# Performance work log

Hardware: AMD Instinct MI355X
Metric: run time of the kernel (lower is better)

## Reference

```python
import jax, jax.numpy as jnp
import numpy as np
from jax import lax

B, L, T = 16, 512, 128
V, D = 21128, 512


def setup_inputs() -> dict:
    key = jax.random.key(0)
    ks = jax.random.split(key, 24)
    s = 0.05
    p = lambda k, shape: jax.random.normal(k, shape, jnp.float32) * s
    return {
        'document_input_ids': jax.random.randint(ks[0], (B, L), 0, V),
        'summary_input_ids': jax.random.randint(ks[1], (B, T), 0, V),
        'E': p(ks[2], (V, D)),
        'Wih_f': p(ks[3], (4 * D, D)), 'Whh_f': p(ks[4], (4 * D, D)),
        'bih_f': p(ks[5], (4 * D,)), 'bhh_f': p(ks[6], (4 * D,)),
        'Wih_b': p(ks[7], (4 * D, D)), 'Whh_b': p(ks[8], (4 * D, D)),
        'bih_b': p(ks[9], (4 * D,)), 'bhh_b': p(ks[10], (4 * D,)),
        'fc_W': p(ks[11], (D, 2 * D)), 'fc_b': p(ks[12], (D,)),
        'attn_W': p(ks[13], (D, 3 * D)), 'attn_b': p(ks[14], (D,)),
        'v_w': p(ks[15], (D,)),
        'dWih': p(ks[16], (4 * D, 3 * D)),
        'dbih': p(ks[17], (4 * D,)), 'dbhh': p(ks[18], (4 * D,)),
        'dfc_W': p(ks[19], (V, 4 * D)), 'dfc_b': p(ks[20], (V,)),
    }


def _lstm_dir(x, Wih, Whh, bih, bhh, reverse):
    # x: (B, L, Din) -> outputs (B, L, D) plus final hidden (B, D)
    xg = jnp.einsum('bld,gd->blg', x, Wih) + bih + bhh  # precompute input gates

    def step(carry, xt):
        h, c = carry
        g = xt + h @ Whh.T
        i, f, gg, o = jnp.split(g, 4, axis=-1)  # PyTorch gate order i,f,g,o
        i = jax.nn.sigmoid(i); f = jax.nn.sigmoid(f)
        gg = jnp.tanh(gg); o = jax.nn.sigmoid(o)
        c = f * c + i * gg
        h = o * jnp.tanh(c)
        return (h, c), h

    h0 = jnp.zeros((x.shape[0], Whh.shape[1]), x.dtype)
    (hT, _), hs = lax.scan(step, (h0, h0), jnp.swapaxes(xg, 0, 1), reverse=reverse)
    return jnp.swapaxes(hs, 0, 1), hT


def reference(document_input_ids, summary_input_ids, E,
              Wih_f, Whh_f, bih_f, bhh_f,
              Wih_b, Whh_b, bih_b, bhh_b,
              fc_W, fc_b, attn_W, attn_b, v_w,
              dWih, dbih, dbhh, dfc_W, dfc_b):
    # --- encoder (BiLSTM over document; dropout is identity at eval) ---
    emb = E[document_input_ids]                       # (B, L, D)
    enc_f, h_f = _lstm_dir(emb, Wih_f, Whh_f, bih_f, bhh_f, reverse=False)
    enc_b, h_b = _lstm_dir(emb, Wih_b, Whh_b, bih_b, bhh_b, reverse=True)
    enc = jnp.concatenate([enc_f, enc_b], axis=-1)    # (B, L, 2D)
    hidden = jnp.tanh(jnp.concatenate([h_f, h_b], axis=-1) @ fc_W.T + fc_b)  # (B, D)

    # --- Bahdanau attention, computed once (as in the original forward) ---
    bsz, dlen = enc.shape[0], enc.shape[1]
    hrep = jnp.broadcast_to(hidden[:, None, :], (bsz, dlen, hidden.shape[-1]))
    energy = jnp.tanh(jnp.concatenate([hrep, enc], axis=2) @ attn_W.T + attn_b)
    att = energy @ v_w                                 # (B, L)
    mask = document_input_ids != 0
    att = jnp.where(mask, att, jnp.float32(-1e10))
    a = jax.nn.softmax(att, axis=1)
    weighted = jnp.einsum('bl,ble->be', a, enc)        # (B, 2D), constant over steps

    # --- decoder: teacher forcing; d_lstm gets a fresh zero state each step,
    # so all T-1 steps are independent and fully vectorized ---
    toks = summary_input_ids[:, :-1]                   # inputs for t = 1..T-1
    emb_s = E[toks]                                    # (B, T-1, D)
    w_b = jnp.broadcast_to(weighted[:, None, :], (bsz, toks.shape[1], weighted.shape[-1]))
    x = jnp.concatenate([emb_s, w_b], axis=2)          # (B, T-1, 3D)
    g = jnp.einsum('btd,gd->btg', x, dWih) + dbih + dbhh
    i, f, gg, o = jnp.split(g, 4, axis=-1)
    c = jax.nn.sigmoid(i) * jnp.tanh(gg)               # h_prev = c_prev = 0
    h = jax.nn.sigmoid(o) * jnp.tanh(c)                # (B, T-1, D)
    pred = jnp.einsum('btd,vd->btv', jnp.concatenate([h, w_b, emb_s], axis=2), dfc_W) + dfc_b
    logits = jnp.concatenate([jnp.zeros((bsz, 1, pred.shape[-1]), pred.dtype), pred], axis=1)
    logits = jnp.transpose(logits, (0, 2, 1))          # (B, V, T) as in the torch code

    # --- CrossEntropyLoss over all positions (incl. the zero-logit t=0) ---
    logp = jax.nn.log_softmax(logits, axis=1)
    nll = -jnp.take_along_axis(logp, summary_input_ids[:, None, :], axis=1).squeeze(1)
    loss = nll.mean()
    return logits, loss
```

## Files before the change

kernel.cpp:

```cpp
#include <hip/hip_runtime.h>
#include <math.h>

typedef __attribute__((ext_vector_type(8))) short bf16x8;
typedef __attribute__((ext_vector_type(4))) float f32x4;
typedef unsigned int u32;
typedef unsigned short u16;
typedef unsigned long long u64;

#define BB 16
#define LL 512
#define TT 128
#define VV 21128
#define DD 512

__device__ __forceinline__ float b2f(u16 h){ return __uint_as_float(((u32)h) << 16); }
__device__ __forceinline__ u16 f2bf(float x){
    u32 u = __float_as_uint(x);
    return (u16)((u + 0x7fffu + ((u >> 16) & 1u)) >> 16);
}
__device__ __forceinline__ float sigf(float x){ return 1.0f / (1.0f + __expf(-x)); }
__device__ __forceinline__ bf16x8 pack8(float4 a, float4 b){
    bf16x8 r;
    r[0]=(short)f2bf(a.x); r[1]=(short)f2bf(a.y); r[2]=(short)f2bf(a.z); r[3]=(short)f2bf(a.w);
    r[4]=(short)f2bf(b.x); r[5]=(short)f2bf(b.y); r[6]=(short)f2bf(b.z); r[7]=(short)f2bf(b.w);
    return r;
}

__global__ void kz(u32* p, int n){
    int i = blockIdx.x * 256 + threadIdx.x;
    if (i < n) p[i] = 0u;
}

__global__ void k_embed(const int* __restrict__ doc, const float* __restrict__ E,
                        u16* __restrict__ emb2){
    int r = blockIdx.x;
    int lane = threadIdx.x;
    int l = r >> 4, b = r & 15;
    int tok = doc[b * LL + l];
    const float* src = E + (size_t)tok * DD + lane * 8;
    float4 a = *(const float4*)(src);
    float4 c = *(const float4*)(src + 4);
    *(bf16x8*)(emb2 + (size_t)r * DD + lane * 8) = pack8(a, c);
}

template<int MODE>
__global__ __launch_bounds__(256) void k_gemm(
    const u16* __restrict__ A, const float* __restrict__ Bt, void* __restrict__ Out,
    const float* __restrict__ b1, const float* __restrict__ b2, int M, int N, int K)
{
    __shared__ u16 smem[17408];
    u16* sA = smem;
    u16* sB = smem + 128 * 56;
    int tid = threadIdx.x;
    int nb = blockIdx.x, mb = blockIdx.y;
    int wv = tid >> 6, lane = tid & 63;
    int wm = wv >> 1, wn = wv & 1;
    int lrow = lane & 15, quad = lane >> 4;
    f32x4 acc[4][4] = {};
    int kt_n = K >> 5;
    for (int kt = 0; kt < kt_n; ++kt){
        int k0 = kt << 5;
        bf16x8 va[2];
        u64 qb[4];
        #pragma unroll
        for (int h = 0; h < 2; ++h){
            int c = tid + (h << 8);
            int row = c >> 2, c4 = c & 3;
            va[h] = *(const bf16x8*)(A + (size_t)(mb * 128 + row) * K + k0 + c4 * 8);
        }
        #pragma unroll
        for (int h = 0; h < 4; ++h){
            int c = tid + (h << 8);
            int row = c >> 3, seg = c & 7;
            int rb = nb * 128 + row; rb = rb < N ? rb : N - 1;
            float4 v = *(const float4*)(Bt + (size_t)rb * K + k0 + seg * 4);
            qb[h] = (u64)f2bf(v.x) | ((u64)f2bf(v.y) << 16) |
                    ((u64)f2bf(v.z) << 32) | ((u64)f2bf(v.w) << 48);
        }
        __syncthreads();
        #pragma unroll
        for (int h = 0; h < 2; ++h){
            int c = tid + (h << 8);
            int row = c >> 2, c4 = c & 3;
            *(bf16x8*)(sA + row * 56 + c4 * 8) = va[h];
        }
        #pragma unroll
        for (int h = 0; h < 4; ++h){
            int c = tid + (h << 8);
            int row = c >> 3, seg = c & 7;
            *(u64*)(sB + row * 56 + seg * 4) = qb[h];
        }
        __syncthreads();
        bf16x8 af[4], bfr[4];
        #pragma unroll
        for (int i = 0; i < 4; ++i){
            af[i]  = *(const bf16x8*)(sA + (wm * 64 + i * 16 + lrow) * 56 + quad * 8);
            bfr[i] = *(const bf16x8*)(sB + (wn * 64 + i * 16 + lrow) * 56 + quad * 8);
        }
        #pragma unroll
        for (int i = 0; i < 4; ++i)
            #pragma unroll
            for (int j = 0; j < 4; ++j)
                acc[i][j] = __builtin_amdgcn_mfma_f32_16x16x32_bf16(af[i], bfr[j], acc[i][j], 0, 0, 0);
    }

    if (MODE == 0 || MODE == 1){
        u16* O = (u16*)Out;
        #pragma unroll
        for (int i = 0; i < 4; ++i){
            int rowb = mb * 128 + wm * 64 + i * 16 + quad * 4;
            #pragma unroll
            for (int j = 0; j < 4; ++j){
                int col = nb * 128 + wn * 64 + j * 16 + lrow;
                float bias = b1[col] + (b2 ? b2[col] : 0.0f);
                #pragma unroll
                for (int r = 0; r < 4; ++r){
                    float v = acc[i][j][r] + bias;
                    if (MODE == 1) v = tanhf(v);
                    O[(size_t)(rowb + r) * N + col] = f2bf(v);
                }
            }
        }
    } else {
        float* Of = (float*)Out;
        float* lds_f = (float*)smem;
        #pragma unroll
        for (int h = 0; h < 2; ++h){
            __syncthreads();
            if (wn == h){
                #pragma unroll
                for (int j = 0; j < 4; ++j){
                    int nl = j * 16 + lrow;
                    int vg = nb * 128 + h * 64 + nl;
                    float bias = (vg < VV) ? b1[vg] : 0.0f;
                    #pragma unroll
                    for (int i = 0; i < 4; ++i){
                        #pragma unroll
                        for (int r = 0; r < 4; ++r){
                            int tl = wm * 64 + i * 16 + quad * 4 + r;
                            lds_f[nl * 132 + tl] = (tl == 0) ? 0.0f : (acc[i][j][r] + bias);
                        }
                    }
                }
            }
            __syncthreads();
            int vloc = tid >> 2, seg = tid & 3;
            int ng = nb * 128 + h * 64 + vloc;
            if (ng < VV){
                float4* dst = (float4*)(Of + ((size_t)mb * VV + ng) * TT + seg * 32);
                const float4* src = (const float4*)(lds_f + vloc * 132 + seg * 32);
                #pragma unroll
                for (int q = 0; q < 8; ++q) dst[q] = src[q];
            }
        }
    }
}

__global__ __launch_bounds__(256) void k_lstm(
    const u16* __restrict__ xg_f, const u16* __restrict__ xg_b,
    const float* __restrict__ Whh_f, const float* __restrict__ Whh_b,
    u16* __restrict__ hist_f, u16* __restrict__ hist_b,
    u32* __restrict__ hbuf, u32* __restrict__ cnt)
{
    __shared__ u16 h_lds[16 * 544];
    __shared__ float g_lds[4 * 16 * 16];
    int tid = threadIdx.x;
    int dir = blockIdx.x >> 5;
    int slice = blockIdx.x & 31;
    int d0 = slice << 4;
    int wv = tid >> 6, lane = tid & 63;
    int lrow = lane & 15, quad = lane >> 4;
    const u16* xg  = dir ? xg_b : xg_f;
    const float* Whh = dir ? Whh_b : Whh_f;
    u16* hist = dir ? hist_b : hist_f;

    bf16x8 bfrag[16];
    {
        int nrow = (wv << 9) + d0 + lrow;
        const float* wp = Whh + (size_t)nrow * DD;
        #pragma unroll
        for (int kb = 0; kb < 16; ++kb){
            float4 x0 = *(const float4*)(wp + kb * 32 + quad * 8);
            float4 x1 = *(const float4*)(wp + kb * 32 + quad * 8 + 4);
            bfrag[kb] = pack8(x0, x1);
        }
    }
    float c_reg = 0.0f;
    int um = tid >> 4, udc = tid & 15;

    for (int s = 0; s < LL; ++s){
        int t = dir ? (LL - 1 - s) : s;
        int rp = s & 1, wpar = rp ^ 1;
        u32* hb_r = hbuf + ((dir * 2 + rp) << 12);
        #pragma unroll
        for (int j = 0; j < 16; ++j){
            u32 u = __hip_atomic_load(hb_r + (j << 8) + tid, __ATOMIC_RELAXED, __HIP_MEMORY_SCOPE_AGENT);
            *(u32*)(h_lds + j * 544 + (tid << 1)) = u;
        }
        __syncthreads();
        f32x4 acc = {};
        #pragma unroll
        for (int kb = 0; kb < 16; ++kb){
            bf16x8 af = *(const bf16x8*)(h_lds + lrow * 544 + kb * 32 + quad * 8);
            acc = __builtin_amdgcn_mfma_f32_16x16x32_bf16(af, bfrag[kb], acc, 0, 0, 0);
        }
        {
            const u16* xp = xg + ((size_t)(t << 4)) * 2048 + (wv << 9) + d0 + lrow;
            #pragma unroll
            for (int r = 0; r < 4; ++r){
                int m = (quad << 2) + r;
                float gv = acc[r] + b2f(xp[(size_t)m * 2048]);
                g_lds[(wv << 8) + (m << 4) + lrow] = gv;
            }
        }
        __syncthreads();
        {
            float gi = g_lds[(0 << 8) + (um << 4) + udc];
            float gf = g_lds[(1 << 8) + (um << 4) + udc];
            float gg = g_lds[(2 << 8) + (um << 4) + udc];
            float go = g_lds[(3 << 8) + (um << 4) + udc];
            float cv = sigf(gf) * c_reg + sigf(gi) * tanhf(gg);
            c_reg = cv;
            float h = sigf(go) * tanhf(cv);
            float ho = __shfl_xor(h, 1);
            if ((tid & 1) == 0){
                u32 u = ((u32)f2bf(ho) << 16) | (u32)f2bf(h);
                u32* hb_w = hbuf + ((dir * 2 + wpar) << 12);
                __hip_atomic_store(hb_w + (um << 8) + ((d0 + udc) >> 1), u, __ATOMIC_RELAXED, __HIP_MEMORY_SCOPE_AGENT);
                *(u32*)(hist + ((size_t)(t * 16 + um)) * DD + d0 + udc) = u;
            }
        }
        __syncthreads();
        if (tid == 0){
            __hip_atomic_fetch_add(cnt, 1, __ATOMIC_ACQ_REL, __HIP_MEMORY_SCOPE_AGENT);
            int target = (s + 1) << 6;
            while (__hip_atomic_load(cnt, __ATOMIC_ACQUIRE, __HIP_MEMORY_SCOPE_AGENT) < target)
                __builtin_amdgcn_s_sleep(2);
        }
        __syncthreads();
    }
}

__global__ void k_fc(const u16* __restrict__ hist_f, const u16* __restrict__ hist_b,
                     const float* __restrict__ fcW, const float* __restrict__ fcB,
                     u16* __restrict__ hidden){
    int idx = blockIdx.x * 256 + threadIdx.x;
    int b = idx >> 9, n = idx & 511;
    const u16* hf = hist_f + (size_t)(511 * 16 + b) * DD;
    const u16* hb = hist_b + (size_t)b * DD;
    const float* w = fcW + (size_t)n * 1024;
    float sacc = 0.0f;
    for (int k = 0; k < 512; ++k) sacc += b2f(hf[k]) * w[k];
    for (int k = 0; k < 512; ++k) sacc += b2f(hb[k]) * w[512 + k];
    hidden[b * 512 + n] = f2bf(tanhf(sacc + fcB[n]));
}

__global__ void k_packatt(const u16* __restrict__ hidden, const u16* __restrict__ hist_f,
                          const u16* __restrict__ hist_b, u16* __restrict__ X){
    int r = blockIdx.x;
    int b = r >> 9, l = r & 511;
    u16* xr = X + (size_t)r * 1536;
    const u16* hf = hist_f + (size_t)(l * 16 + b) * DD;
    const u16* hb = hist_b + (size_t)(l * 16 + b) * DD;
    const u16* hd = hidden + b * 512;
    for (int j = threadIdx.x; j < 512; j += 256){
        xr[j] = hd[j];
        xr[512 + j] = hf[j];
        xr[1024 + j] = hb[j];
    }
}

__global__ void k_att(const u16* __restrict__ energy, const float* __restrict__ vw,
                      const int* __restrict__ doc, float* __restrict__ att){
    int r = blockIdx.x * 4 + (threadIdx.x >> 6);
    int lane = threadIdx.x & 63;
    bf16x8 e = *(const bf16x8*)(energy + (size_t)r * 512 + lane * 8);
    float4 v0 = *(const float4*)(vw + lane * 8);
    float4 v1 = *(const float4*)(vw + lane * 8 + 4);
    float sacc = b2f((u16)e[0]) * v0.x + b2f((u16)e[1]) * v0.y +
                 b2f((u16)e[2]) * v0.z + b2f((u16)e[3]) * v0.w +
                 b2f((u16)e[4]) * v1.x + b2f((u16)e[5]) * v1.y +
                 b2f((u16)e[6]) * v1.z + b2f((u16)e[7]) * v1.w;
    #pragma unroll
    for (int o = 1; o < 64; o <<= 1) sacc += __shfl_xor(sacc, o);
    if (lane == 0){
        int b = r >> 9, l = r & 511;
        att[r] = (doc[b * 512 + l] != 0) ? sacc : -1e10f;
    }
}

__global__ __launch_bounds__(256) void k_smw(const float* __restrict__ att,
                                             const u16* __restrict__ hist_f,
                                             const u16* __restrict__ hist_b,
                                             float* __restrict__ weighted){
    __shared__ float sa[512];
    __shared__ float red[256];
    int b = blockIdx.x, tid = threadIdx.x;
    float a0 = att[b * 512 + tid], a1 = att[b * 512 + 256 + tid];
    red[tid] = fmaxf(a0, a1); __syncthreads();
    for (int o = 128; o > 0; o >>= 1){ if (tid < o) red[tid] = fmaxf(red[tid], red[tid + o]); __syncthreads(); }
    float mx = red[0]; __syncthreads();
    float e0 = __expf(a0 - mx), e1 = __expf(a1 - mx);
    red[tid] = e0 + e1; __syncthreads();
    for (int o = 128; o > 0; o >>= 1){ if (tid < o) red[tid] += red[tid + o]; __syncthreads(); }
    float inv = 1.0f / red[0];
    sa[tid] = e0 * inv; sa[256 + tid] = e1 * inv;
    __syncthreads();
    #pragma unroll
    for (int ch = 0; ch < 4; ++ch){
        int e = (ch << 8) + tid;
        const u16* src = (e < 512) ? (hist_f + b * DD + e) : (hist_b + b * DD + (e - 512));
        float acc = 0.0f;
        for (int l = 0; l < 512; ++l) acc += sa[l] * b2f(src[(size_t)l * 16 * DD]);
        weighted[b * 1024 + e] = acc;
    }
}

__global__ void k_packdec(const int* __restrict__ sids, const float* __restrict__ E,
                          const float* __restrict__ weighted,
                          u16* __restrict__ X_dec, u16* __restrict__ X_pred){
    int r = blockIdx.x;
    int b = r >> 7, t = r & 127;
    u16* xd = X_dec + (size_t)r * 1536;
    u16* xp = X_pred + (size_t)r * 2048;
    const float* er = (t > 0) ? (E + (size_t)sids[b * 128 + t - 1] * DD) : (const float*)0;
    for (int j = threadIdx.x; j < 512; j += 256){
        u16 v = (t > 0) ? f2bf(er[j]) : (u16)0;
        xd[j] = v; xp[1536 + j] = v;
    }
    for (int j = threadIdx.x; j < 1024; j += 256){
        u16 wv = f2bf(weighted[b * 1024 + j]);
        xd[512 + j] = wv; xp[512 + j] = wv;
    }
}

__global__ void k_gate(const u16* __restrict__ g, u16* __restrict__ X_pred){
    int idx = blockIdx.x * 256 + threadIdx.x;
    int r = idx >> 9, d = idx & 511;
    const u16* gr = g + (size_t)r * 2048;
    float gi = b2f(gr[d]), gg = b2f(gr[1024 + d]), go = b2f(gr[1536 + d]);
    float c = sigf(gi) * tanhf(gg);
    X_pred[(size_t)r * 2048 + d] = f2bf(sigf(go) * tanhf(c));
}

__global__ void k_lossp(const float* __restrict__ out, float* __restrict__ part){
    int b = blockIdx.x >> 5, ch = blockIdx.x & 31;
    int t = threadIdx.x;
    int v0 = ch * 661, v1 = v0 + 661; if (v1 > VV) v1 = VV;
    const float* col = out + (size_t)b * VV * TT + t;
    float m = -1e30f, sacc = 0.0f;
    for (int v = v0; v < v1; ++v){
        float x = col[(size_t)v * TT];
        float nm = fmaxf(m, x);
        sacc = sacc * __expf(m - nm) + __expf(x - nm);
        m = nm;
    }
    float2* p = (float2*)part;
    p[((b * 32 + ch) << 7) + t] = make_float2(m, sacc);
}

__global__ __launch_bounds__(256) void k_lossm(const float* __restrict__ part,
                                               const float* __restrict__ out,
                                               const int* __restrict__ sids,
                                               float* __restrict__ loss_out){
    __shared__ float red[256];
    int tid = threadIdx.x;
    float local = 0.0f;
    #pragma unroll
    for (int p8 = 0; p8 < 8; ++p8){
        int pair = (p8 << 8) + tid;
        int b = pair >> 7, t = pair & 127;
        const float2* pp = (const float2*)part + ((size_t)(b * 32) << 7) + t;
        float M = -1e30f;
        for (int c = 0; c < 32; ++c) M = fmaxf(M, pp[c << 7].x);
        float S = 0.0f;
        for (int c = 0; c < 32; ++c){ float2 q = pp[c << 7]; S += q.y * __expf(q.x - M); }
        float logZ = M + __logf(S);
        int tgt = sids[b * 128 + t];
        float x = out[(size_t)b * VV * TT + (size_t)tgt * TT + t];
        local += (logZ - x);
    }
    red[tid] = local; __syncthreads();
    for (int o = 128; o > 0; o >>= 1){ if (tid < o) red[tid] += red[tid + o]; __syncthreads(); }
    if (tid == 0) loss_out[0] = red[0] / 2048.0f;
}

extern "C" void kernel_launch(void* const* d_in, const int* in_sizes, int n_in,
                              void* d_out, int out_size, void* d_ws, size_t ws_size,
                              hipStream_t stream)
{
    const int*   doc  = (const int*)d_in[0];
    const int*   sids = (const int*)d_in[1];
    const float* E    = (const float*)d_in[2];
    const float* WihF = (const float*)d_in[3];
    const float* WhhF = (const float*)d_in[4];
    const float* bihF = (const float*)d_in[5];
    const float* bhhF = (const float*)d_in[6];
    const float* WihB = (const float*)d_in[7];
    const float* WhhB = (const float*)d_in[8];
    const float* bihB = (const float*)d_in[9];
    const float* bhhB = (const float*)d_in[10];
    const float* fcW  = (const float*)d_in[11];
    const float* fcB  = (const float*)d_in[12];
    const float* attW = (const float*)d_in[13];
    const float* attB = (const float*)d_in[14];
    const float* vw   = (const float*)d_in[15];
    const float* dWih = (const float*)d_in[16];
    const float* dbih = (const float*)d_in[17];
    const float* dbhh = (const float*)d_in[18];
    const float* dfcW = (const float*)d_in[19];
    const float* dfcB = (const float*)d_in[20];
    float* out = (float*)d_out;

    char* ws = (char*)d_ws;
    const size_t EMB2 = 0;
    const size_t XG   = EMB2 + 8388608ull;
    const size_t XGB  = XG   + 33554432ull;
    const size_t HHF  = XGB  + 33554432ull;
    const size_t HHB  = HHF  + 8388608ull;
    const size_t HBUF = HHB  + 8388608ull;
    const size_t HID  = HBUF + 66560ull;
    const size_t XATT = XG;
    const size_t ENER = XATT + 25165824ull;
    const size_t ATT  = ENER + 8388608ull;
    const size_t WEI  = ATT  + 32768ull;
    const size_t XDEC = WEI  + 65536ull;
    const size_t GDEC = XDEC + 6291456ull;
    const size_t XPRD = GDEC + 8388608ull;
    const size_t PART = XPRD + 8388608ull;

    u16* emb2  = (u16*)(ws + EMB2);
    u16* xgf   = (u16*)(ws + XG);
    u16* xgb   = (u16*)(ws + XGB);
    u16* hhf   = (u16*)(ws + HHF);
    u16* hhb   = (u16*)(ws + HHB);
    u32* hbuf  = (u32*)(ws + HBUF);
    u16* hid   = (u16*)(ws + HID);
    u16* xatt  = (u16*)(ws + XATT);
    u16* ener  = (u16*)(ws + ENER);
    float* att = (float*)(ws + ATT);
    float* wei = (float*)(ws + WEI);
    u16* xdec  = (u16*)(ws + XDEC);
    u16* gdec  = (u16*)(ws + GDEC);
    u16* xprd  = (u16*)(ws + XPRD);
    float* part= (float*)(ws + PART);

    (void)in_sizes; (void)n_in; (void)out_size; (void)ws_size;

    kz<<<dim3(65), dim3(256), 0, stream>>>(hbuf, 16512);
    k_embed<<<dim3(8192), dim3(64), 0, stream>>>(doc, E, emb2);
    k_gemm<0><<<dim3(16, 64), dim3(256), 0, stream>>>(emb2, WihF, (void*)xgf, bihF, bhhF, 8192, 2048, 512);
    k_gemm<0><<<dim3(16, 64), dim3(256), 0, stream>>>(emb2, WihB, (void*)xgb, bihB, bhhB, 8192, 2048, 512);
    k_lstm<<<dim3(64), dim3(256), 0, stream>>>(xgf, xgb, WhhF, WhhB, hhf, hhb, hbuf, hbuf + 16384);
    k_fc<<<dim3(32), dim3(256), 0, stream>>>(hhf, hhb, fcW, fcB, hid);
    k_packatt<<<dim3(8192), dim3(256), 0, stream>>>(hid, hhf, hhb, xatt);
    k_gemm<1><<<dim3(4, 64), dim3(256), 0, stream>>>(xatt, attW, (void*)ener, attB, (const float*)0, 8192, 512, 1536);
    k_att<<<dim3(2048), dim3(256), 0, stream>>>(ener, vw, doc, att);
    k_smw<<<dim3(16), dim3(256), 0, stream>>>(att, hhf, hhb, wei);
    k_packdec<<<dim3(2048), dim3(256), 0, stream>>>(sids, E, wei, xdec, xprd);
    k_gemm<0><<<dim3(16, 16), dim3(256), 0, stream>>>(xdec, dWih, (void*)gdec, dbih, dbhh, 2048, 2048, 1536);
    k_gate<<<dim3(4096), dim3(256), 0, stream>>>(gdec, xprd);
    k_gemm<2><<<dim3(166, 16), dim3(256), 0, stream>>>(xprd, dfcW, (void*)out, dfcB, (const float*)0, 2048, 21128, 2048);
    k_lossp<<<dim3(512), dim3(128), 0, stream>>>(out, part);
    k_lossm<<<dim3(1), dim3(256), 0, stream>>>(part, out, sids, out + (size_t)BB * VV * TT);
}
```

Baseline: 5.472 ms.

## Restructure LSTM recurrence into per-wave slices with flag-based point-to-point sync

The recurrent LSTM kernel now gives each wave all four gates of a 16-column hidden slice, keeping the four recurrent weight fragments in registers. This removes the LDS staging of gates and the block-level barriers. The global atomic counter barrier is replaced by per-wave release flags that every wave polls with acquire loads, and h is read straight from global memory into MFMA fragments. The xg loads are issued before the wait so their latency overlaps it. The trade-off is higher register pressure (64 bf16x8 weight fragments per lane) and only 16 blocks, with each wave polling 32 flags per step.

```diff
diff --git a/kernel.cpp b/kernel.cpp
--- a/kernel.cpp
+++ b/kernel.cpp
@@ -156,88 +156,100 @@
     }
 }
 
-__global__ __launch_bounds__(256) void k_lstm(
+__global__ __launch_bounds__(256, 1) void k_lstm(
     const u16* __restrict__ xg_f, const u16* __restrict__ xg_b,
     const float* __restrict__ Whh_f, const float* __restrict__ Whh_b,
     u16* __restrict__ hist_f, u16* __restrict__ hist_b,
-    u32* __restrict__ hbuf, u32* __restrict__ cnt)
+    u32* __restrict__ hbuf, u32* __restrict__ flags)
 {
-    __shared__ u16 h_lds[16 * 544];
-    __shared__ float g_lds[4 * 16 * 16];
     int tid = threadIdx.x;
-    int dir = blockIdx.x >> 5;
-    int slice = blockIdx.x & 31;
-    int d0 = slice << 4;
     int wv = tid >> 6, lane = tid & 63;
+    int blk = blockIdx.x;
+    int dir = blk >> 3;
+    int w = ((blk & 7) << 2) + wv;
+    int d0 = w << 4;
     int lrow = lane & 15, quad = lane >> 4;
+
     const u16* xg  = dir ? xg_b : xg_f;
     const float* Whh = dir ? Whh_b : Whh_f;
     u16* hist = dir ? hist_b : hist_f;
-
-    bf16x8 bfrag[16];
-    {
-        int nrow = (wv << 9) + d0 + lrow;
-        const float* wp = Whh + (size_t)nrow * DD;
+    u32* myflag = flags + (((dir << 5) + w) << 5);
+    u32* pflag  = flags + (((dir << 5) + (lane & 31)) << 5);
+
+    bf16x8 bfr[4][16];
+    #pragma unroll
+    for (int g = 0; g < 4; ++g){
+        const float* wp = Whh + (size_t)((g << 9) + d0 + lrow) * DD;
         #pragma unroll
         for (int kb = 0; kb < 16; ++kb){
             float4 x0 = *(const float4*)(wp + kb * 32 + quad * 8);
             float4 x1 = *(const float4*)(wp + kb * 32 + quad * 8 + 4);
-            bfrag[kb] = pack8(x0, x1);
-        }
-    }
-    float c_reg = 0.0f;
-    int um = tid >> 4, udc = tid & 15;
+            bfr[g][kb] = pack8(x0, x1);
+        }
+    }
+    float c_reg[4] = {0.0f, 0.0f, 0.0f, 0.0f};
 
     for (int s = 0; s < LL; ++s){
         int t = dir ? (LL - 1 - s) : s;
-        int rp = s & 1, wpar = rp ^ 1;
+        int rp = s & 1;
         u32* hb_r = hbuf + ((dir * 2 + rp) << 12);
-        #pragma unroll
-        for (int j = 0; j < 16; ++j){
-            u32 u = __hip_atomic_load(hb_r + (j << 8) + tid, __ATOMIC_RELAXED, __HIP_MEMORY_SCOPE_AGENT);
-            *(u32*)(h_lds + j * 544 + (tid << 1)) = u;
-        }
-        __syncthreads();
-        f32x4 acc = {};
+        u32* hb_w = hbuf + ((dir * 2 + (rp ^ 1)) << 12);
+
+        u16 xv[4][4];
+        const u16* xgp = xg + (size_t)(t << 4) * 2048 + d0 + lrow;
+        #pragma unroll
+        for (int g = 0; g < 4; ++g)
+            #pragma unroll
+            for (int r = 0; r < 4; ++r)
+                xv[g][r] = xgp[(size_t)((quad << 2) + r) * 2048 + (g << 9)];
+
+        if (s){
+            u32 tgt = (u32)s;
+            while (1){
+                u32 v = __hip_atomic_load(pflag, __ATOMIC_ACQUIRE, __HIP_MEMORY_SCOPE_AGENT);
+                if (__all((int)(v >= tgt))) break;
+                __builtin_amdgcn_s_sleep(1);
+            }
+        }
+
+        u64* hrow = (u64*)(hb_r + (lrow << 8));
+        bf16x8 af[16];
         #pragma unroll
         for (int kb = 0; kb < 16; ++kb){
-            bf16x8 af = *(const bf16x8*)(h_lds + lrow * 544 + kb * 32 + quad * 8);
-            acc = __builtin_amdgcn_mfma_f32_16x16x32_bf16(af, bfrag[kb], acc, 0, 0, 0);
-        }
-        {
-            const u16* xp = xg + ((size_t)(t << 4)) * 2048 + (wv << 9) + d0 + lrow;
+            union { u64 q[2]; bf16x8 v; } u;
+            u.q[0] = __hip_atomic_load(hrow + kb * 8 + quad * 2,     __ATOMIC_RELAXED, __HIP_MEMORY_SCOPE_AGENT);
+            u.q[1] = __hip_atomic_load(hrow + kb * 8 + quad * 2 + 1, __ATOMIC_RELAXED, __HIP_MEMORY_SCOPE_AGENT);
+            af[kb] = u.v;
+        }
+
+        f32x4 acc[4] = {};
+        #pragma unroll
+        for (int kb = 0; kb < 16; ++kb){
             #pragma unroll
-            for (int r = 0; r < 4; ++r){
-                int m = (quad << 2) + r;
-                float gv = acc[r] + b2f(xp[(size_t)m * 2048]);
-                g_lds[(wv << 8) + (m << 4) + lrow] = gv;
+            for (int g = 0; g < 4; ++g)
+                acc[g] = __builtin_amdgcn_mfma_f32_16x16x32_bf16(af[kb], bfr[g][kb], acc[g], 0, 0, 0);
+        }
+
+        #pragma unroll
+        for (int r = 0; r < 4; ++r){
+            float gi = acc[0][r] + b2f(xv[0][r]);
+            float gf = acc[1][r] + b2f(xv[1][r]);
+            float gg = acc[2][r] + b2f(xv[2][r]);
+            float go = acc[3][r] + b2f(xv[3][r]);
+            float cv = sigf(gf) * c_reg[r] + sigf(gi) * tanhf(gg);
+            c_reg[r] = cv;
+            u32 me = (u32)f2bf(sigf(go) * tanhf(cv));
+            u32 ot = __shfl_xor(me, 1);
+            if (!(lane & 1)){
+                u32 uw = me | (ot << 16);
+                int batch = (quad << 2) + r;
+                __hip_atomic_store(hb_w + (batch << 8) + ((d0 + lrow) >> 1), uw,
+                                   __ATOMIC_RELAXED, __HIP_MEMORY_SCOPE_AGENT);
+                *(u32*)(hist + (size_t)((t << 4) + batch) * DD + d0 + lrow) = uw;
             }
         }
-        __syncthreads();
-        {
-            float gi = g_lds[(0 << 8) + (um << 4) + udc];
-            float gf = g_lds[(1 << 8) + (um << 4) + udc];
-            float gg = g_lds[(2 << 8) + (um << 4) + udc];
-            float go = g_lds[(3 << 8) + (um << 4) + udc];
-            float cv = sigf(gf) * c_reg + sigf(gi) * tanhf(gg);
-            c_reg = cv;
-            float h = sigf(go) * tanhf(cv);
-            float ho = __shfl_xor(h, 1);
-            if ((tid & 1) == 0){
-                u32 u = ((u32)f2bf(ho) << 16) | (u32)f2bf(h);
-                u32* hb_w = hbuf + ((dir * 2 + wpar) << 12);
-                __hip_atomic_store(hb_w + (um << 8) + ((d0 + udc) >> 1), u, __ATOMIC_RELAXED, __HIP_MEMORY_SCOPE_AGENT);
-                *(u32*)(hist + ((size_t)(t * 16 + um)) * DD + d0 + udc) = u;
-            }
-        }
-        __syncthreads();
-        if (tid == 0){
-            __hip_atomic_fetch_add(cnt, 1, __ATOMIC_ACQ_REL, __HIP_MEMORY_SCOPE_AGENT);
-            int target = (s + 1) << 6;
-            while (__hip_atomic_load(cnt, __ATOMIC_ACQUIRE, __HIP_MEMORY_SCOPE_AGENT) < target)
-                __builtin_amdgcn_s_sleep(2);
-        }
-        __syncthreads();
+        if (lane == 0)
+            __hip_atomic_store(myflag, (u32)(s + 1), __ATOMIC_RELEASE, __HIP_MEMORY_SCOPE_AGENT);
     }
 }
 
@@ -420,6 +432,7 @@
     const size_t HHB  = HHF  + 8388608ull;
     const size_t HBUF = HHB  + 8388608ull;
     const size_t HID  = HBUF + 66560ull;
+    const size_t FLG  = 0;
     const size_t XATT = XG;
     const size_t ENER = XATT + 25165824ull;
     const size_t ATT  = ENER + 8388608ull;
@@ -435,6 +448,7 @@
     u16* hhf   = (u16*)(ws + HHF);
     u16* hhb   = (u16*)(ws + HHB);
     u32* hbuf  = (u32*)(ws + HBUF);
+    u32* flags = (u32*)(ws + FLG);
     u16* hid   = (u16*)(ws + HID);
     u16* xatt  = (u16*)(ws + XATT);
     u16* ener  = (u16*)(ws + ENER);
@@ -447,11 +461,12 @@
 
     (void)in_sizes; (void)n_in; (void)out_size; (void)ws_size;
 
-    kz<<<dim3(65), dim3(256), 0, stream>>>(hbuf, 16512);
+    kz<<<dim3(64), dim3(256), 0, stream>>>(hbuf, 16384);
     k_embed<<<dim3(8192), dim3(64), 0, stream>>>(doc, E, emb2);
     k_gemm<0><<<dim3(16, 64), dim3(256), 0, stream>>>(emb2, WihF, (void*)xgf, bihF, bhhF, 8192, 2048, 512);
     k_gemm<0><<<dim3(16, 64), dim3(256), 0, stream>>>(emb2, WihB, (void*)xgb, bihB, bhhB, 8192, 2048, 512);
-    k_lstm<<<dim3(64), dim3(256), 0, stream>>>(xgf, xgb, WhhF, WhhB, hhf, hhb, hbuf, hbuf + 16384);
+    kz<<<dim3(8), dim3(256), 0, stream>>>(flags, 2048);
+    k_lstm<<<dim3(16), dim3(256), 0, stream>>>(xgf, xgb, WhhF, WhhB, hhf, hhb, hbuf, flags);
     k_fc<<<dim3(32), dim3(256), 0, stream>>>(hhf, hhb, fcW, fcB, hid);
     k_packatt<<<dim3(8192), dim3(256), 0, stream>>>(hid, hhf, hhb, xatt);
     k_gemm<1><<<dim3(4, 64), dim3(256), 0, stream>>>(xatt, attW, (void*)ener, attB, (const float*)0, 8192, 512, 1536);
```

Result: slower. 5.759 ms (+5.3%).
